# Performance work log

Measured on AMD Instinct MI355X. Metric: run time of the kernel, lower is better.

## Reference

```python
import jax, jax.numpy as jnp
import numpy as np

T = 4          # spiking time steps
HEADS = 12
SCALE = 0.125
TAU = 2.0
ALPHA = 4.0    # sigmoid surrogate sharpness
EPS = 1e-5

@jax.custom_vjp
def spike(x):
    # Heaviside forward, sigmoid surrogate backward (SigmoidGrad)
    return (x > 0).astype(x.dtype)

def _spike_fwd(x):
    return (x > 0).astype(x.dtype), x

def _spike_bwd(x, g):
    s = jax.nn.sigmoid(ALPHA * x)
    return (g * ALPHA * s * (1.0 - s),)

spike.defvjp(_spike_fwd, _spike_bwd)

def lif(x, threshold):
    # layer-by-layer LIF: x is [T*B, ...]; scan membrane over T steps
    TB = x.shape[0]
    B = TB // T
    xt = x.reshape((T, B) + x.shape[1:])
    def step(mem, xi):
        mem = mem + (xi - mem) / TAU
        s = spike(mem - threshold)
        mem = mem * (1.0 - jax.lax.stop_gradient(s))  # hard reset, spike detached
        return mem, s
    _, sp = jax.lax.scan(step, jnp.zeros_like(xt[0]), xt)
    return sp.reshape(x.shape)

def bn(x, p):
    # inference BatchNorm; p = [gamma, beta, mean, var] each [C], channel axis 1
    shape = (1, x.shape[1]) + (1,) * (x.ndim - 2)
    inv = jax.lax.rsqrt(p[3] + EPS)
    return (x - p[2].reshape(shape)) * (p[0] * inv).reshape(shape) + p[1].reshape(shape)

def setup_inputs() -> dict:
    key = jax.random.key(0)
    ks = jax.random.split(key, 9)
    C, HID, TB, H = 384, 1536, 128, 14
    return {
        'x': jax.random.normal(ks[0], (TB, C, H, H), jnp.float32),
        'qkvp_w': jax.random.normal(ks[1], (4, C, C), jnp.float32) * 0.05,
        'qkvp_bn': jax.random.uniform(ks[2], (4, 4, C), jnp.float32),
        'fc1_w': jax.random.normal(ks[3], (HID, C), jnp.float32) * 0.05,
        'fc1_b': jax.random.normal(ks[4], (HID,), jnp.float32) * 0.05,
        'fc1_bn': jax.random.uniform(ks[5], (4, HID), jnp.float32),
        'fc2_w': jax.random.normal(ks[6], (C, HID), jnp.float32) * 0.05,
        'fc2_b': jax.random.normal(ks[7], (C,), jnp.float32) * 0.05,
        'fc2_bn': jax.random.uniform(ks[8], (4, C), jnp.float32),
    }

def reference(x, qkvp_w, qkvp_bn, fc1_w, fc1_b, fc1_bn, fc2_w, fc2_b, fc2_bn):
    TB, C, H, W = x.shape
    N = H * W
    d = C // HEADS
    xf = x.reshape(TB, C, N)

    def branch(i):
        y = jnp.einsum('oc,bcn->bon', qkvp_w[i], xf)  # conv1d k=1, no bias
        y = lif(bn(y, qkvp_bn[i]), 1.0)
        # [TB,C,N] -> [TB,N,C] -> [TB,N,heads,d] -> [TB,heads,N,d]
        return y.transpose(0, 2, 1).reshape(TB, N, HEADS, d).transpose(0, 2, 1, 3)

    q, k, v = branch(0), branch(1), branch(2)
    attn = jnp.einsum('bhqd,bhkd->bhqk', q, k) * SCALE  # no softmax (spiking SSA)
    o = jnp.einsum('bhqk,bhkd->bhqd', attn, v)
    o = o.transpose(0, 1, 3, 2).reshape(TB, C, N)       # head-major channel layout
    o = lif(o, 0.5)                                     # attn_lif threshold=0.5
    o = jnp.einsum('oc,bcn->bon', qkvp_w[3], o)         # proj conv
    o = lif(bn(o, qkvp_bn[3]), 1.0).reshape(TB, C, H, W)

    x = x + o                                           # attention residual

    h = jnp.einsum('oc,bchw->bohw', fc1_w, x) + fc1_b[None, :, None, None]
    h = lif(bn(h, fc1_bn), 1.0)
    h = jnp.einsum('oc,bchw->bohw', fc2_w, h) + fc2_b[None, :, None, None]
    h = lif(bn(h, fc2_bn), 1.0)

    x = x + h                                           # MLP residual
    return (x, v)
```

## Files before the change

### kernel.cpp

```cpp
#include <hip/hip_runtime.h>
#include <hip/hip_bf16.h>


#define Cv 384
#define Nv 196
#define Mv 25088
#define HIDv 1536
#define Bv 32
#define Zv 6272
#define TBv 128
#define CHUNK 12544
#define UC 3136

__global__ __launch_bounds__(256) void k_transpose_in(const float* __restrict__ x,
                                                      float* __restrict__ xp)
{
    int idx = blockIdx.x * 256 + threadIdx.x;
    int c   = idx / Mv;
    int rem = idx - c * Mv;
    int z = rem >> 2, t = rem & 3;
    int b = z / Nv, n = z - b * Nv;
    xp[idx] = x[((size_t)(t * Bv + b) * Cv + c) * Nv + n];
}

__global__ __launch_bounds__(256) void k_gemm3(const float* __restrict__ W,
                                               const float* __restrict__ X,
                                               float* __restrict__ Y,
                                               int K, int ldx, int ldy,
                                               const float* __restrict__ bias,
                                               int cb)
{
    __shared__ float sW[16][68];
    __shared__ float sX[16][64];
    int ym0 = blockIdx.x * 64;
    int m0  = cb + ym0;
    int o0  = blockIdx.y * 64;
    int tid = threadIdx.x;
    int wo = tid & 63, wh = tid >> 6;
    int xr = tid >> 4, xc = (tid & 15) * 4;
    int to = tid >> 4, tm = tid & 15;

    const float* Wp = W + (size_t)(o0 + wo) * K + wh * 4;
    const float* Xp = X + (size_t)xr * ldx + m0 + xc;

    float acc[4][4];
    #pragma unroll
    for (int i = 0; i < 4; ++i)
        #pragma unroll
        for (int j = 0; j < 4; ++j) acc[i][j] = 0.0f;

    for (int k0 = 0; k0 < K; k0 += 16) {
        float4 w4 = *(const float4*)(Wp + k0);
        float4 x4 = *(const float4*)(Xp + (size_t)k0 * ldx);
        __syncthreads();
        sW[wh*4+0][wo] = w4.x;
        sW[wh*4+1][wo] = w4.y;
        sW[wh*4+2][wo] = w4.z;
        sW[wh*4+3][wo] = w4.w;
        *(float4*)&sX[xr][xc] = x4;
        __syncthreads();
        #pragma unroll
        for (int kk = 0; kk < 16; ++kk) {
            float4 a = *(const float4*)&sW[kk][to*4];
            float4 b = *(const float4*)&sX[kk][tm*4];
            float av[4] = {a.x, a.y, a.z, a.w};
            float bv[4] = {b.x, b.y, b.z, b.w};
            #pragma unroll
            for (int i = 0; i < 4; ++i)
                #pragma unroll
                for (int j = 0; j < 4; ++j)
                    acc[i][j] = fmaf(av[i], bv[j], acc[i][j]);
        }
    }
    #pragma unroll
    for (int i = 0; i < 4; ++i) {
        int o = o0 + to*4 + i;
        float bb = bias ? bias[o] : 0.0f;
        float4 r;
        r.x = acc[i][0] + bb; r.y = acc[i][1] + bb;
        r.z = acc[i][2] + bb; r.w = acc[i][3] + bb;
        *(float4*)&Y[(size_t)o * ldy + ym0 + tm*4] = r;
    }
}

__global__ __launch_bounds__(256) void k_vsse2(const float* __restrict__ W,
                                               const float* __restrict__ X,
                                               const float* __restrict__ bnp,
                                               __hip_bfloat16* __restrict__ Y)
{
    __shared__ float sW[32][68];
    __shared__ float sX[32][64];
    int m0 = blockIdx.x * 64;
    int o0 = blockIdx.y * 64;
    int tid = threadIdx.x;
    int to = tid >> 4, tm = tid & 15;

    float acc[4][4][4];
    #pragma unroll
    for (int s = 0; s < 4; ++s)
        #pragma unroll
        for (int op = 0; op < 4; ++op)
            #pragma unroll
            for (int e = 0; e < 4; ++e) acc[s][op][e] = 0.0f;

    int wq_o = tid >> 3, wq_c = tid & 7;
    int xs_r = tid >> 3, xs_c = (tid & 7) * 8;

    for (int blk = 0; blk < 12; ++blk) {
        int k0 = blk * 32;
        __syncthreads();
        {
            float4 w4 = *(const float4*)(W + (size_t)(o0 + wq_o) * Cv + k0 + wq_c*4);
            sW[wq_c*4+0][wq_o] = w4.x;
            sW[wq_c*4+1][wq_o] = w4.y;
            sW[wq_c*4+2][wq_o] = w4.z;
            sW[wq_c*4+3][wq_o] = w4.w;
            float4 w5 = *(const float4*)(W + (size_t)(o0 + 32 + wq_o) * Cv + k0 + wq_c*4);
            sW[wq_c*4+0][32 + wq_o] = w5.x;
            sW[wq_c*4+1][32 + wq_o] = w5.y;
            sW[wq_c*4+2][32 + wq_o] = w5.z;
            sW[wq_c*4+3][32 + wq_o] = w5.w;
        }
        {
            const float* Xp = X + (size_t)(k0 + xs_r) * Mv + m0 + xs_c;
            *(float4*)&sX[xs_r][xs_c]     = *(const float4*)(Xp);
            *(float4*)&sX[xs_r][xs_c + 4] = *(const float4*)(Xp + 4);
        }
        __syncthreads();
        #pragma unroll
        for (int j = 0; j < 8; ++j) {
            #pragma unroll
            for (int s = 0; s < 4; ++s) {
                int kk = j * 4 + s;
                float4 w4 = *(const float4*)&sW[kk][to*4];
                float4 x4 = *(const float4*)&sX[kk][tm*4];
                float wv[4] = {w4.x, w4.y, w4.z, w4.w};
                float xv[4] = {x4.x, x4.y, x4.z, x4.w};
                #pragma unroll
                for (int op = 0; op < 4; ++op)
                    #pragma unroll
                    for (int e = 0; e < 4; ++e)
                        acc[s][op][e] = __fadd_rn(acc[s][op][e],
                                                  __fmul_rn(wv[op], xv[e]));
            }
        }
    }

    #pragma unroll
    for (int op = 0; op < 4; ++op) {
        int o = o0 + to*4 + op;
        float inv = __fdiv_rn(1.0f, __fsqrt_rn(__fadd_rn(bnp[3*Cv + o], 1e-5f)));
        float sc  = __fmul_rn(bnp[o], inv);
        float mu  = bnp[2*Cv + o];
        float be  = bnp[Cv + o];
        float mem = 0.0f;
        ushort4 pk;
        unsigned short* pks = (unsigned short*)&pk;
        #pragma unroll
        for (int e = 0; e < 4; ++e) {
            float tot = __fadd_rn(__fadd_rn(acc[0][op][e], acc[2][op][e]),
                                  __fadd_rn(acc[1][op][e], acc[3][op][e]));
            float bn = __fadd_rn(__fmul_rn(__fsub_rn(tot, mu), sc), be);
            mem = __fadd_rn(mem, __fmul_rn(__fsub_rn(bn, mem), 0.5f));
            int s = (mem > 1.0f);
            mem = s ? 0.0f : mem;
            pks[e] = s ? 0x3F80 : 0;
        }
        *(ushort4*)((unsigned short*)Y + (size_t)o * Mv + m0 + tm * 4) = pk;
    }
}

__global__ __launch_bounds__(256) void k_bnlif_spike(const float* __restrict__ y,
                                                     const float* __restrict__ bnp,
                                                     __hip_bfloat16* __restrict__ sp)
{
    int idx = blockIdx.x * 256 + threadIdx.x;
    int c = idx / Zv;
    float gamma = bnp[c], beta = bnp[Cv+c], mean = bnp[2*Cv+c], var = bnp[3*Cv+c];
    float scale = gamma / sqrtf(var + 1e-5f);
    size_t base = (size_t)idx * 4;
    float4 yv = *(const float4*)(y + base);
    float xi[4] = {yv.x, yv.y, yv.z, yv.w};
    ushort4 pk;
    unsigned short* pks = (unsigned short*)&pk;
    float mem = 0.f;
    #pragma unroll
    for (int t = 0; t < 4; ++t) {
        float xv = (xi[t] - mean) * scale + beta;
        mem = mem + (xv - mem) * 0.5f;
        float s = (mem > 1.0f) ? 1.0f : 0.0f;
        mem *= (1.0f - s);
        pks[t] = (s > 0.5f) ? 0x3F80 : 0;
    }
    *(ushort4*)((unsigned short*)sp + base) = pk;
}

__global__ __launch_bounds__(256) void k_attn(const __hip_bfloat16* __restrict__ qs,
                                              const __hip_bfloat16* __restrict__ ks,
                                              const __hip_bfloat16* __restrict__ vs,
                                              float* __restrict__ o_chan,
                                              float* __restrict__ v_out)
{
    int h = blockIdx.x, tbl = blockIdx.y;
    int t = tbl >> 5, b = tbl & 31;
    int tid = threadIdx.x;
    __shared__ unsigned kmask[196];
    __shared__ float vf[196][36];
    size_t chb  = (size_t)h * 32 * Mv;
    size_t colb = (size_t)b * Nv * 4 + t;

    for (int e = tid; e < Nv * 32; e += 256) {
        int dd = e / Nv, n = e - dd * Nv;
        vf[n][dd] = __bfloat162float(vs[chb + (size_t)dd * Mv + colb + (size_t)n * 4]);
    }
    unsigned qm = 0;
    if (tid < Nv) {
        unsigned km = 0;
        #pragma unroll
        for (int dd = 0; dd < 32; ++dd) {
            size_t off = chb + (size_t)dd * Mv + colb + (size_t)tid * 4;
            km |= (__bfloat162float(ks[off]) > 0.5f ? 1u : 0u) << dd;
            qm |= (__bfloat162float(qs[off]) > 0.5f ? 1u : 0u) << dd;
        }
        kmask[tid] = km;
    }
    __syncthreads();
    for (int e = tid; e < Nv * 32; e += 256) {
        int n = e >> 5, dd = e & 31;
        v_out[((size_t)(tbl * 12 + h) * Nv + n) * 32 + dd] = vf[n][dd];
    }
    if (tid < Nv) {
        float acc[32] = {};
        for (int nk = 0; nk < Nv; ++nk) {
            float a = (float)__popc(qm & kmask[nk]) * 0.125f;
            #pragma unroll
            for (int dd = 0; dd < 32; ++dd) acc[dd] += a * vf[nk][dd];
        }
        #pragma unroll
        for (int dd = 0; dd < 32; ++dd)
            o_chan[chb + (size_t)dd * Mv + colb + (size_t)tid * 4] = acc[dd];
    }
}

__global__ __launch_bounds__(256) void k_attnlif(float* __restrict__ o)
{
    int idx = blockIdx.x * 256 + threadIdx.x;
    size_t base = (size_t)idx * 4;
    float4 v = *(const float4*)(o + base);
    float xi[4] = {v.x, v.y, v.z, v.w};
    float s4[4];
    float mem = 0.f;
    #pragma unroll
    for (int t = 0; t < 4; ++t) {
        mem = mem + (xi[t] - mem) * 0.5f;
        s4[t] = (mem > 0.5f) ? 1.0f : 0.0f;
        mem *= (1.0f - s4[t]);
    }
    float4 r; r.x = s4[0]; r.y = s4[1]; r.z = s4[2]; r.w = s4[3];
    *(float4*)(o + base) = r;
}

__global__ __launch_bounds__(256) void k_resid(const float* __restrict__ p,
                                               const float* __restrict__ bnp,
                                               float* __restrict__ x1,
                                               __hip_bfloat16* __restrict__ s_proj)
{
    int idx = blockIdx.x * 256 + threadIdx.x;
    int c = idx / Zv;
    float gamma = bnp[c], beta = bnp[Cv+c], mean = bnp[2*Cv+c], var = bnp[3*Cv+c];
    float scale = gamma / sqrtf(var + 1e-5f);
    size_t base = (size_t)idx * 4;
    float4 pv = *(const float4*)(p + base);
    float xi[4] = {pv.x, pv.y, pv.z, pv.w};
    float4 xv = *(const float4*)(x1 + base);
    float xr[4] = {xv.x, xv.y, xv.z, xv.w};
    ushort4 pk;
    unsigned short* pks = (unsigned short*)&pk;
    float mem = 0.f;
    #pragma unroll
    for (int t = 0; t < 4; ++t) {
        float bnv = (xi[t] - mean) * scale + beta;
        mem = mem + (bnv - mem) * 0.5f;
        float s = (mem > 1.0f) ? 1.0f : 0.0f;
        mem *= (1.0f - s);
        xr[t] += s;
        pks[t] = (s > 0.5f) ? 0x3F80 : 0;
    }
    float4 r; r.x = xr[0]; r.y = xr[1]; r.z = xr[2]; r.w = xr[3];
    *(float4*)(x1 + base) = r;
    *(ushort4*)((unsigned short*)s_proj + base) = pk;
}

__global__ __launch_bounds__(256) void k_bnlif_h(float* __restrict__ hbuf,
                                                 const float* __restrict__ bnp)
{
    int idx = blockIdx.x * 256 + threadIdx.x;
    int o = idx / UC;
    float gamma = bnp[o], beta = bnp[HIDv+o], mean = bnp[2*HIDv+o], var = bnp[3*HIDv+o];
    float scale = gamma / sqrtf(var + 1e-5f);
    size_t base = (size_t)idx * 4;
    float4 hv = *(const float4*)(hbuf + base);
    float xi[4] = {hv.x, hv.y, hv.z, hv.w};
    float s4[4];
    float mem = 0.f;
    #pragma unroll
    for (int t = 0; t < 4; ++t) {
        float bnv = (xi[t] - mean) * scale + beta;
        mem = mem + (bnv - mem) * 0.5f;
        s4[t] = (mem > 1.0f) ? 1.0f : 0.0f;
        mem *= (1.0f - s4[t]);
    }
    float4 r; r.x = s4[0]; r.y = s4[1]; r.z = s4[2]; r.w = s4[3];
    *(float4*)(hbuf + base) = r;
}

__global__ __launch_bounds__(256) void k_final(const float* __restrict__ h2,
                                               const float* __restrict__ bnp,
                                               const float* __restrict__ x,
                                               const __hip_bfloat16* __restrict__ s_proj,
                                               float* __restrict__ out,
                                               int b0)
{
    int idx = blockIdx.x * 256 + threadIdx.x;
    int c = idx / UC;
    int u = idx - c * UC;
    int bp = u / Nv, n = u - bp * Nv;
    int b = b0 + bp;
    float gamma = bnp[c], beta = bnp[Cv+c], mean = bnp[2*Cv+c], var = bnp[3*Cv+c];
    float scale = gamma / sqrtf(var + 1e-5f);
    float4 hv = *(const float4*)(h2 + (size_t)c * CHUNK + (size_t)u * 4);
    float xi[4] = {hv.x, hv.y, hv.z, hv.w};
    ushort4 sp4 = *(const ushort4*)((const unsigned short*)s_proj +
                                    (size_t)c * Mv + ((size_t)b * Nv + n) * 4);
    unsigned short* sps = (unsigned short*)&sp4;
    float mem = 0.f;
    #pragma unroll
    for (int t = 0; t < 4; ++t) {
        float bnv = (xi[t] - mean) * scale + beta;
        mem = mem + (bnv - mem) * 0.5f;
        float s = (mem > 1.0f) ? 1.0f : 0.0f;
        mem *= (1.0f - s);
        size_t oidx = ((size_t)(t * Bv + b) * Cv + c) * Nv + n;
        float sproj = sps[t] ? 1.0f : 0.0f;
        out[oidx] = x[oidx] + sproj + s;
    }
}

extern "C" void kernel_launch(void* const* d_in, const int* in_sizes, int n_in,
                              void* d_out, int out_size, void* d_ws, size_t ws_size,
                              hipStream_t stream)
{
    const float* x       = (const float*)d_in[0];
    const float* qkvp_w  = (const float*)d_in[1];
    const float* qkvp_bn = (const float*)d_in[2];
    const float* fc1_w   = (const float*)d_in[3];
    const float* fc1_b   = (const float*)d_in[4];
    const float* fc1_bn  = (const float*)d_in[5];
    const float* fc2_w   = (const float*)d_in[6];
    const float* fc2_b   = (const float*)d_in[7];
    const float* fc2_bn  = (const float*)d_in[8];

    float* out1 = (float*)d_out;
    float* out2 = out1 + (size_t)TBv * Cv * Nv;

    float* wsf = (float*)d_ws;
    const size_t S = (size_t)Cv * Mv;
    if (ws_size < 4 * S * sizeof(float)) return;

    float* xp   = wsf;
    float* ybuf = wsf + S;
    __hip_bfloat16* qs = (__hip_bfloat16*)(wsf + 2*S);
    __hip_bfloat16* ks = qs + S;
    __hip_bfloat16* vs = qs + 2*S;
    float* pbuf  = wsf + 2*S;
    float* hbuf  = wsf + S;
    float* h2buf = wsf + 3*S;
    __hip_bfloat16* s_proj = (__hip_bfloat16*)(wsf + 3*S + S/2);

    k_transpose_in<<<37632, 256, 0, stream>>>(x, xp);

    for (int br = 0; br < 2; ++br) {
        k_gemm3<<<dim3(392, 6), 256, 0, stream>>>(qkvp_w + (size_t)br*Cv*Cv, xp, ybuf,
                                                  Cv, Mv, Mv, nullptr, 0);
        __hip_bfloat16* sp = (br == 0) ? qs : ks;
        k_bnlif_spike<<<9408, 256, 0, stream>>>(ybuf, qkvp_bn + (size_t)br*4*Cv, sp);
    }
    k_vsse2<<<dim3(392, 6), 256, 0, stream>>>(qkvp_w + (size_t)2*Cv*Cv, xp,
                                              qkvp_bn + (size_t)2*4*Cv, vs);

    k_attn<<<dim3(12, 128), 256, 0, stream>>>(qs, ks, vs, ybuf, out2);
    k_attnlif<<<9408, 256, 0, stream>>>(ybuf);

    k_gemm3<<<dim3(392, 6), 256, 0, stream>>>(qkvp_w + (size_t)3*Cv*Cv, ybuf, pbuf,
                                              Cv, Mv, Mv, nullptr, 0);
    k_resid<<<9408, 256, 0, stream>>>(pbuf, qkvp_bn + (size_t)3*4*Cv, xp, s_proj);

    for (int ch = 0; ch < 2; ++ch) {
        k_gemm3<<<dim3(196, 24), 256, 0, stream>>>(fc1_w, xp, hbuf,
                                                   Cv, Mv, CHUNK, fc1_b, ch * CHUNK);
        k_bnlif_h<<<18816, 256, 0, stream>>>(hbuf, fc1_bn);
        k_gemm3<<<dim3(196, 6), 256, 0, stream>>>(fc2_w, hbuf, h2buf,
                                                  HIDv, CHUNK, CHUNK, fc2_b, 0);
        k_final<<<4704, 256, 0, stream>>>(h2buf, fc2_bn, x, s_proj, out1, ch * 16);
    }
}
```

Baseline: 1.450 ms.

## Fuse fc1 with BN+LIF into bf16 spikes, widen GEMM tiles, drop MLP chunking

Replaces the 64x64 fp32 GEMM with a 64x128 tile variant that can read bf16 inputs. fc1 now applies bias, BatchNorm and LIF in its epilogue and writes bf16 spikes directly. This removes the separate bnlif pass and the full fp32 hidden-activation round trip. With the smaller hidden buffer the MLP runs in one pass instead of two chunks, and the workspace layout is reorganised to fit. The larger accumulator tile raises register pressure and may lower occupancy.

```diff
diff --git a/kernel.cpp b/kernel.cpp
--- a/kernel.cpp
+++ b/kernel.cpp
@@ -9,8 +9,6 @@
 #define Bv 32
 #define Zv 6272
 #define TBv 128
-#define CHUNK 12544
-#define UC 3136
 
 __global__ __launch_bounds__(256) void k_transpose_in(const float* __restrict__ x,
                                                       float* __restrict__ xp)
@@ -23,52 +21,70 @@
     xp[idx] = x[((size_t)(t * Bv + b) * Cv + c) * Nv + n];
 }
 
-__global__ __launch_bounds__(256) void k_gemm3(const float* __restrict__ W,
-                                               const float* __restrict__ X,
+template<int XBF16>
+__global__ __launch_bounds__(256) void k_gemm4(const float* __restrict__ W,
+                                               const void* __restrict__ Xv,
                                                float* __restrict__ Y,
                                                int K, int ldx, int ldy,
                                                const float* __restrict__ bias,
                                                int cb)
 {
     __shared__ float sW[16][68];
-    __shared__ float sX[16][64];
-    int ym0 = blockIdx.x * 64;
+    __shared__ float sX[16][128];
+    int ym0 = blockIdx.x * 128;
     int m0  = cb + ym0;
     int o0  = blockIdx.y * 64;
     int tid = threadIdx.x;
     int wo = tid & 63, wh = tid >> 6;
-    int xr = tid >> 4, xc = (tid & 15) * 4;
+    int xr = tid >> 4, xc = (tid & 15) * 8;
     int to = tid >> 4, tm = tid & 15;
 
     const float* Wp = W + (size_t)(o0 + wo) * K + wh * 4;
-    const float* Xp = X + (size_t)xr * ldx + m0 + xc;
-
-    float acc[4][4];
+
+    float acc[4][8];
     #pragma unroll
     for (int i = 0; i < 4; ++i)
         #pragma unroll
-        for (int j = 0; j < 4; ++j) acc[i][j] = 0.0f;
+        for (int j = 0; j < 8; ++j) acc[i][j] = 0.0f;
 
     for (int k0 = 0; k0 < K; k0 += 16) {
         float4 w4 = *(const float4*)(Wp + k0);
-        float4 x4 = *(const float4*)(Xp + (size_t)k0 * ldx);
+        float xf[8];
+        if (XBF16) {
+            const unsigned short* Xb = (const unsigned short*)Xv;
+            uint4 u = *(const uint4*)(Xb + (size_t)(k0 + xr) * ldx + m0 + xc);
+            unsigned uu[4] = {u.x, u.y, u.z, u.w};
+            #pragma unroll
+            for (int q = 0; q < 4; ++q) {
+                xf[2*q]   = __uint_as_float((uu[q] & 0xFFFFu) << 16);
+                xf[2*q+1] = __uint_as_float(uu[q] & 0xFFFF0000u);
+            }
+        } else {
+            const float* Xf = (const float*)Xv;
+            float4 xa = *(const float4*)(Xf + (size_t)(k0 + xr) * ldx + m0 + xc);
+            float4 xb = *(const float4*)(Xf + (size_t)(k0 + xr) * ldx + m0 + xc + 4);
+            xf[0]=xa.x; xf[1]=xa.y; xf[2]=xa.z; xf[3]=xa.w;
+            xf[4]=xb.x; xf[5]=xb.y; xf[6]=xb.z; xf[7]=xb.w;
+        }
         __syncthreads();
         sW[wh*4+0][wo] = w4.x;
         sW[wh*4+1][wo] = w4.y;
         sW[wh*4+2][wo] = w4.z;
         sW[wh*4+3][wo] = w4.w;
-        *(float4*)&sX[xr][xc] = x4;
+        *(float4*)&sX[xr][xc]     = *(float4*)&xf[0];
+        *(float4*)&sX[xr][xc + 4] = *(float4*)&xf[4];
         __syncthreads();
         #pragma unroll
         for (int kk = 0; kk < 16; ++kk) {
-            float4 a = *(const float4*)&sW[kk][to*4];
-            float4 b = *(const float4*)&sX[kk][tm*4];
+            float4 a  = *(const float4*)&sW[kk][to*4];
+            float4 b0 = *(const float4*)&sX[kk][tm*4];
+            float4 b1 = *(const float4*)&sX[kk][64 + tm*4];
             float av[4] = {a.x, a.y, a.z, a.w};
-            float bv[4] = {b.x, b.y, b.z, b.w};
+            float bv[8] = {b0.x,b0.y,b0.z,b0.w,b1.x,b1.y,b1.z,b1.w};
             #pragma unroll
             for (int i = 0; i < 4; ++i)
                 #pragma unroll
-                for (int j = 0; j < 4; ++j)
+                for (int j = 0; j < 8; ++j)
                     acc[i][j] = fmaf(av[i], bv[j], acc[i][j]);
         }
     }
@@ -76,10 +92,88 @@
     for (int i = 0; i < 4; ++i) {
         int o = o0 + to*4 + i;
         float bb = bias ? bias[o] : 0.0f;
-        float4 r;
-        r.x = acc[i][0] + bb; r.y = acc[i][1] + bb;
-        r.z = acc[i][2] + bb; r.w = acc[i][3] + bb;
-        *(float4*)&Y[(size_t)o * ldy + ym0 + tm*4] = r;
+        float4 r0, r1;
+        r0.x = acc[i][0] + bb; r0.y = acc[i][1] + bb;
+        r0.z = acc[i][2] + bb; r0.w = acc[i][3] + bb;
+        r1.x = acc[i][4] + bb; r1.y = acc[i][5] + bb;
+        r1.z = acc[i][6] + bb; r1.w = acc[i][7] + bb;
+        *(float4*)&Y[(size_t)o * ldy + ym0 + tm*4]      = r0;
+        *(float4*)&Y[(size_t)o * ldy + ym0 + 64 + tm*4] = r1;
+    }
+}
+
+__global__ __launch_bounds__(256) void k_fc1(const float* __restrict__ W,
+                                             const float* __restrict__ X,
+                                             const float* __restrict__ bias,
+                                             const float* __restrict__ bnp,
+                                             __hip_bfloat16* __restrict__ H)
+{
+    __shared__ float sW[16][68];
+    __shared__ float sX[16][128];
+    int ym0 = blockIdx.x * 128;
+    int o0  = blockIdx.y * 64;
+    int tid = threadIdx.x;
+    int wo = tid & 63, wh = tid >> 6;
+    int xr = tid >> 4, xc = (tid & 15) * 8;
+    int to = tid >> 4, tm = tid & 15;
+
+    const float* Wp = W + (size_t)(o0 + wo) * Cv + wh * 4;
+
+    float acc[4][8];
+    #pragma unroll
+    for (int i = 0; i < 4; ++i)
+        #pragma unroll
+        for (int j = 0; j < 8; ++j) acc[i][j] = 0.0f;
+
+    for (int k0 = 0; k0 < Cv; k0 += 16) {
+        float4 w4 = *(const float4*)(Wp + k0);
+        float4 xa = *(const float4*)(X + (size_t)(k0 + xr) * Mv + ym0 + xc);
+        float4 xb = *(const float4*)(X + (size_t)(k0 + xr) * Mv + ym0 + xc + 4);
+        __syncthreads();
+        sW[wh*4+0][wo] = w4.x;
+        sW[wh*4+1][wo] = w4.y;
+        sW[wh*4+2][wo] = w4.z;
+        sW[wh*4+3][wo] = w4.w;
+        *(float4*)&sX[xr][xc]     = xa;
+        *(float4*)&sX[xr][xc + 4] = xb;
+        __syncthreads();
+        #pragma unroll
+        for (int kk = 0; kk < 16; ++kk) {
+            float4 a  = *(const float4*)&sW[kk][to*4];
+            float4 b0 = *(const float4*)&sX[kk][tm*4];
+            float4 b1 = *(const float4*)&sX[kk][64 + tm*4];
+            float av[4] = {a.x, a.y, a.z, a.w};
+            float bv[8] = {b0.x,b0.y,b0.z,b0.w,b1.x,b1.y,b1.z,b1.w};
+            #pragma unroll
+            for (int i = 0; i < 4; ++i)
+                #pragma unroll
+                for (int j = 0; j < 8; ++j)
+                    acc[i][j] = fmaf(av[i], bv[j], acc[i][j]);
+        }
+    }
+    #pragma unroll
+    for (int i = 0; i < 4; ++i) {
+        int o = o0 + to*4 + i;
+        float inv = __fdiv_rn(1.0f, __fsqrt_rn(__fadd_rn(bnp[3*HIDv + o], 1e-5f)));
+        float sc  = __fmul_rn(bnp[o], inv);
+        float mu  = bnp[2*HIDv + o];
+        float be  = bnp[HIDv + o];
+        #pragma unroll
+        for (int half = 0; half < 2; ++half) {
+            float mem = 0.0f;
+            ushort4 pk;
+            unsigned short* pks = (unsigned short*)&pk;
+            #pragma unroll
+            for (int t = 0; t < 4; ++t) {
+                float val = __fadd_rn(acc[i][half*4 + t], bias[o]);
+                float bn  = __fadd_rn(__fmul_rn(__fsub_rn(val, mu), sc), be);
+                mem = __fadd_rn(mem, __fmul_rn(__fsub_rn(bn, mem), 0.5f));
+                int s = (mem > 1.0f);
+                mem = s ? 0.0f : mem;
+                pks[t] = s ? 0x3F80 : 0;
+            }
+            *(ushort4*)((unsigned short*)H + (size_t)o * Mv + ym0 + half*64 + tm*4) = pk;
+        }
     }
 }
 
@@ -291,47 +385,22 @@
     *(ushort4*)((unsigned short*)s_proj + base) = pk;
 }
 
-__global__ __launch_bounds__(256) void k_bnlif_h(float* __restrict__ hbuf,
-                                                 const float* __restrict__ bnp)
-{
-    int idx = blockIdx.x * 256 + threadIdx.x;
-    int o = idx / UC;
-    float gamma = bnp[o], beta = bnp[HIDv+o], mean = bnp[2*HIDv+o], var = bnp[3*HIDv+o];
-    float scale = gamma / sqrtf(var + 1e-5f);
-    size_t base = (size_t)idx * 4;
-    float4 hv = *(const float4*)(hbuf + base);
-    float xi[4] = {hv.x, hv.y, hv.z, hv.w};
-    float s4[4];
-    float mem = 0.f;
-    #pragma unroll
-    for (int t = 0; t < 4; ++t) {
-        float bnv = (xi[t] - mean) * scale + beta;
-        mem = mem + (bnv - mem) * 0.5f;
-        s4[t] = (mem > 1.0f) ? 1.0f : 0.0f;
-        mem *= (1.0f - s4[t]);
-    }
-    float4 r; r.x = s4[0]; r.y = s4[1]; r.z = s4[2]; r.w = s4[3];
-    *(float4*)(hbuf + base) = r;
-}
-
 __global__ __launch_bounds__(256) void k_final(const float* __restrict__ h2,
                                                const float* __restrict__ bnp,
                                                const float* __restrict__ x,
                                                const __hip_bfloat16* __restrict__ s_proj,
-                                               float* __restrict__ out,
-                                               int b0)
+                                               float* __restrict__ out)
 {
     int idx = blockIdx.x * 256 + threadIdx.x;
-    int c = idx / UC;
-    int u = idx - c * UC;
-    int bp = u / Nv, n = u - bp * Nv;
-    int b = b0 + bp;
+    int c = idx / Zv;
+    int z = idx - c * Zv;
+    int b = z / Nv, n = z - b * Nv;
     float gamma = bnp[c], beta = bnp[Cv+c], mean = bnp[2*Cv+c], var = bnp[3*Cv+c];
     float scale = gamma / sqrtf(var + 1e-5f);
-    float4 hv = *(const float4*)(h2 + (size_t)c * CHUNK + (size_t)u * 4);
+    size_t base = (size_t)idx * 4;
+    float4 hv = *(const float4*)(h2 + base);
     float xi[4] = {hv.x, hv.y, hv.z, hv.w};
-    ushort4 sp4 = *(const ushort4*)((const unsigned short*)s_proj +
-                                    (size_t)c * Mv + ((size_t)b * Nv + n) * 4);
+    ushort4 sp4 = *(const ushort4*)((const unsigned short*)s_proj + base);
     unsigned short* sps = (unsigned short*)&sp4;
     float mem = 0.f;
     #pragma unroll
@@ -363,44 +432,43 @@
     float* out1 = (float*)d_out;
     float* out2 = out1 + (size_t)TBv * Cv * Nv;
 
-    float* wsf = (float*)d_ws;
-    const size_t S = (size_t)Cv * Mv;
-    if (ws_size < 4 * S * sizeof(float)) return;
-
-    float* xp   = wsf;
-    float* ybuf = wsf + S;
-    __hip_bfloat16* qs = (__hip_bfloat16*)(wsf + 2*S);
-    __hip_bfloat16* ks = qs + S;
-    __hip_bfloat16* vs = qs + 2*S;
-    float* pbuf  = wsf + 2*S;
-    float* hbuf  = wsf + S;
-    float* h2buf = wsf + 3*S;
-    __hip_bfloat16* s_proj = (__hip_bfloat16*)(wsf + 3*S + S/2);
-
-    k_transpose_in<<<37632, 256, 0, stream>>>(x, xp);
+    const size_t S  = (size_t)Cv * Mv;
+    const size_t S4 = S * 4;
+    if (ws_size < 4 * S4) return;
+
+    char* wb = (char*)d_ws;
+    float* xp            = (float*)wb;
+    float* ybuf          = (float*)(wb + S4);
+    __hip_bfloat16* qs   = (__hip_bfloat16*)(wb + 2*S4);
+    __hip_bfloat16* ks   = (__hip_bfloat16*)(wb + 2*S4 + S4/2);
+    __hip_bfloat16* vs   = (__hip_bfloat16*)(wb + 3*S4);
+    float* pbuf          = (float*)(wb + 2*S4);
+    __hip_bfloat16* s_pr = (__hip_bfloat16*)(wb + 3*S4 + S4/2);
+    __hip_bfloat16* H    = (__hip_bfloat16*)(wb + S4);
+    float* h2            = (float*)wb;
+
+    k_transpose_in<<<(int)(S/256), 256, 0, stream>>>(x, xp);
 
     for (int br = 0; br < 2; ++br) {
-        k_gemm3<<<dim3(392, 6), 256, 0, stream>>>(qkvp_w + (size_t)br*Cv*Cv, xp, ybuf,
-                                                  Cv, Mv, Mv, nullptr, 0);
+        k_gemm4<0><<<dim3(196, 6), 256, 0, stream>>>(qkvp_w + (size_t)br*Cv*Cv, xp,
+                                                     ybuf, Cv, Mv, Mv, nullptr, 0);
         __hip_bfloat16* sp = (br == 0) ? qs : ks;
-        k_bnlif_spike<<<9408, 256, 0, stream>>>(ybuf, qkvp_bn + (size_t)br*4*Cv, sp);
+        k_bnlif_spike<<<(int)(S/1024), 256, 0, stream>>>(ybuf, qkvp_bn + (size_t)br*4*Cv, sp);
     }
     k_vsse2<<<dim3(392, 6), 256, 0, stream>>>(qkvp_w + (size_t)2*Cv*Cv, xp,
                                               qkvp_bn + (size_t)2*4*Cv, vs);
 
     k_attn<<<dim3(12, 128), 256, 0, stream>>>(qs, ks, vs, ybuf, out2);
-    k_attnlif<<<9408, 256, 0, stream>>>(ybuf);
-
-    k_gemm3<<<dim3(392, 6), 256, 0, stream>>>(qkvp_w + (size_t)3*Cv*Cv, ybuf, pbuf,
-                                              Cv, Mv, Mv, nullptr, 0);
-    k_resid<<<9408, 256, 0, stream>>>(pbuf, qkvp_bn + (size_t)3*4*Cv, xp, s_proj);
-
-    for (int ch = 0; ch < 2; ++ch) {
-        k_gemm3<<<dim3(196, 24), 256, 0, stream>>>(fc1_w, xp, hbuf,
-                                                   Cv, Mv, CHUNK, fc1_b, ch * CHUNK);
-        k_bnlif_h<<<18816, 256, 0, stream>>>(hbuf, fc1_bn);
-        k_gemm3<<<dim3(196, 6), 256, 0, stream>>>(fc2_w, hbuf, h2buf,
-                                                  HIDv, CHUNK, CHUNK, fc2_b, 0);
-        k_final<<<4704, 256, 0, stream>>>(h2buf, fc2_bn, x, s_proj, out1, ch * 16);
-    }
-}
+    k_attnlif<<<(int)(S/1024), 256, 0, stream>>>(ybuf);
+
+    k_gemm4<0><<<dim3(196, 6), 256, 0, stream>>>(qkvp_w + (size_t)3*Cv*Cv, ybuf,
+                                                 pbuf, Cv, Mv, Mv, nullptr, 0);
+    k_resid<<<(int)(S/1024), 256, 0, stream>>>(pbuf, qkvp_bn + (size_t)3*4*Cv, xp, s_pr);
+
+    k_fc1<<<dim3(196, 24), 256, 0, stream>>>(fc1_w, xp, fc1_b, fc1_bn, H);
+
+    k_gemm4<1><<<dim3(196, 6), 256, 0, stream>>>(fc2_w, H, h2,
+                                                 HIDv, Mv, Mv, fc2_b, 0);
+
+    k_final<<<(int)(S/1024), 256, 0, stream>>>(h2, fc2_bn, x, s_pr, out1);
+}
```

Measured after the change: 1.366 ms. -5.8%, faster.

## Fuse BN+LIF epilogues into a templated GEMM and drop intermediate elementwise kernels

Applied to the files above, without the earlier changes.

Replaces the shared-memory tiled GEMM with a templated kernel that stages only X in LDS, reads W per wavefront from global/scalar memory, and applies BN+LIF spiking directly in the epilogue, writing bf16 spikes. The separate bnlif, resid and bnlif_h kernels go away: the attention residual is folded into the fc1 GEMM's input load, and the fc1 hidden activations are stored as bf16 spikes that fc2 reads. The MLP no longer runs in two chunks. This cuts full-tensor fp32 round trips and launches. The cost is that W is read through uniform per-wave loads instead of LDS, which may be less efficient.

```diff
diff --git a/kernel.cpp b/kernel.cpp
--- a/kernel.cpp
+++ b/kernel.cpp
@@ -9,8 +9,6 @@
 #define Bv 32
 #define Zv 6272
 #define TBv 128
-#define CHUNK 12544
-#define UC 3136
 
 __global__ __launch_bounds__(256) void k_transpose_in(const float* __restrict__ x,
                                                       float* __restrict__ xp)
@@ -23,63 +21,108 @@
     xp[idx] = x[((size_t)(t * Bv + b) * Cv + c) * Nv + n];
 }
 
-__global__ __launch_bounds__(256) void k_gemm3(const float* __restrict__ W,
-                                               const float* __restrict__ X,
-                                               float* __restrict__ Y,
-                                               int K, int ldx, int ldy,
+template<int XBF16, int SADD, int BIAS, int EPI>
+__global__ __launch_bounds__(256) void k_gemm5(const float* __restrict__ W,
+                                               const void* __restrict__ Xv,
+                                               const __hip_bfloat16* __restrict__ Xs,
                                                const float* __restrict__ bias,
-                                               int cb)
-{
-    __shared__ float sW[16][68];
-    __shared__ float sX[16][64];
-    int ym0 = blockIdx.x * 64;
-    int m0  = cb + ym0;
-    int o0  = blockIdx.y * 64;
-    int tid = threadIdx.x;
-    int wo = tid & 63, wh = tid >> 6;
-    int xr = tid >> 4, xc = (tid & 15) * 4;
-    int to = tid >> 4, tm = tid & 15;
-
-    const float* Wp = W + (size_t)(o0 + wo) * K + wh * 4;
-    const float* Xp = X + (size_t)xr * ldx + m0 + xc;
-
-    float acc[4][4];
-    #pragma unroll
-    for (int i = 0; i < 4; ++i)
+                                               const float* __restrict__ bnp,
+                                               int bnC,
+                                               void* __restrict__ Y,
+                                               int K)
+{
+    __shared__ float sX[8][256];
+    int tid  = threadIdx.x;
+    int lane = tid & 63;
+    int wid  = __builtin_amdgcn_readfirstlane(tid >> 6);
+    int m0   = blockIdx.x * 256;
+    int ob   = blockIdx.y * 32 + wid * 8;
+    int mL   = m0 + lane * 4;
+    int sr   = tid >> 5;
+    int sc   = (tid & 31) * 8;
+
+    float acc[8][4];
+    #pragma unroll
+    for (int i = 0; i < 8; ++i)
         #pragma unroll
         for (int j = 0; j < 4; ++j) acc[i][j] = 0.0f;
 
-    for (int k0 = 0; k0 < K; k0 += 16) {
-        float4 w4 = *(const float4*)(Wp + k0);
-        float4 x4 = *(const float4*)(Xp + (size_t)k0 * ldx);
+    for (int k0 = 0; k0 < K; k0 += 8) {
+        float xf[8];
+        if (XBF16) {
+            const unsigned short* Xb = (const unsigned short*)Xv;
+            uint4 u = *(const uint4*)(Xb + (size_t)(k0 + sr) * Mv + m0 + sc);
+            unsigned uu[4] = {u.x, u.y, u.z, u.w};
+            #pragma unroll
+            for (int q = 0; q < 4; ++q) {
+                xf[2*q]   = __uint_as_float((uu[q] & 0xFFFFu) << 16);
+                xf[2*q+1] = __uint_as_float(uu[q] & 0xFFFF0000u);
+            }
+        } else {
+            const float* Xf = (const float*)Xv;
+            float4 xa = *(const float4*)(Xf + (size_t)(k0 + sr) * Mv + m0 + sc);
+            float4 xb = *(const float4*)(Xf + (size_t)(k0 + sr) * Mv + m0 + sc + 4);
+            xf[0]=xa.x; xf[1]=xa.y; xf[2]=xa.z; xf[3]=xa.w;
+            xf[4]=xb.x; xf[5]=xb.y; xf[6]=xb.z; xf[7]=xb.w;
+            if (SADD) {
+                uint4 u = *(const uint4*)((const unsigned short*)Xs +
+                                          (size_t)(k0 + sr) * Mv + m0 + sc);
+                unsigned uu[4] = {u.x, u.y, u.z, u.w};
+                #pragma unroll
+                for (int q = 0; q < 4; ++q) {
+                    xf[2*q]   = __fadd_rn(xf[2*q],   (uu[q] & 0xFFFFu)      ? 1.0f : 0.0f);
+                    xf[2*q+1] = __fadd_rn(xf[2*q+1], (uu[q] & 0xFFFF0000u) ? 1.0f : 0.0f);
+                }
+            }
+        }
         __syncthreads();
-        sW[wh*4+0][wo] = w4.x;
-        sW[wh*4+1][wo] = w4.y;
-        sW[wh*4+2][wo] = w4.z;
-        sW[wh*4+3][wo] = w4.w;
-        *(float4*)&sX[xr][xc] = x4;
+        *(float4*)&sX[sr][sc]     = *(float4*)&xf[0];
+        *(float4*)&sX[sr][sc + 4] = *(float4*)&xf[4];
         __syncthreads();
-        #pragma unroll
-        for (int kk = 0; kk < 16; ++kk) {
-            float4 a = *(const float4*)&sW[kk][to*4];
-            float4 b = *(const float4*)&sX[kk][tm*4];
-            float av[4] = {a.x, a.y, a.z, a.w};
-            float bv[4] = {b.x, b.y, b.z, b.w};
-            #pragma unroll
-            for (int i = 0; i < 4; ++i)
+        const float* Wb = W + (size_t)ob * K + k0;
+        #pragma unroll
+        for (int kk = 0; kk < 8; ++kk) {
+            float4 xq = *(const float4*)&sX[kk][lane * 4];
+            float xv[4] = {xq.x, xq.y, xq.z, xq.w};
+            #pragma unroll
+            for (int i = 0; i < 8; ++i) {
+                float wv = Wb[(size_t)i * K + kk];
                 #pragma unroll
                 for (int j = 0; j < 4; ++j)
-                    acc[i][j] = fmaf(av[i], bv[j], acc[i][j]);
-        }
-    }
-    #pragma unroll
-    for (int i = 0; i < 4; ++i) {
-        int o = o0 + to*4 + i;
-        float bb = bias ? bias[o] : 0.0f;
-        float4 r;
-        r.x = acc[i][0] + bb; r.y = acc[i][1] + bb;
-        r.z = acc[i][2] + bb; r.w = acc[i][3] + bb;
-        *(float4*)&Y[(size_t)o * ldy + ym0 + tm*4] = r;
+                    acc[i][j] = fmaf(wv, xv[j], acc[i][j]);
+            }
+        }
+    }
+
+    #pragma unroll
+    for (int i = 0; i < 8; ++i) {
+        int o = ob + i;
+        if (EPI == 0) {
+            float bb = BIAS ? bias[o] : 0.0f;
+            float4 r;
+            r.x = acc[i][0] + bb; r.y = acc[i][1] + bb;
+            r.z = acc[i][2] + bb; r.w = acc[i][3] + bb;
+            *(float4*)((float*)Y + (size_t)o * Mv + mL) = r;
+        } else {
+            float inv = __fdiv_rn(1.0f, __fsqrt_rn(__fadd_rn(bnp[3*bnC + o], 1e-5f)));
+            float scl = __fmul_rn(bnp[o], inv);
+            float mu  = bnp[2*bnC + o];
+            float be  = bnp[bnC + o];
+            float mem = 0.0f;
+            ushort4 pk;
+            unsigned short* pks = (unsigned short*)&pk;
+            #pragma unroll
+            for (int j = 0; j < 4; ++j) {
+                float val = acc[i][j];
+                if (BIAS) val = __fadd_rn(val, bias[o]);
+                float bn = __fadd_rn(__fmul_rn(__fsub_rn(val, mu), scl), be);
+                mem = __fadd_rn(mem, __fmul_rn(__fsub_rn(bn, mem), 0.5f));
+                int s = (mem > 1.0f);
+                mem = s ? 0.0f : mem;
+                pks[j] = s ? 0x3F80 : 0;
+            }
+            *(ushort4*)((unsigned short*)Y + (size_t)o * Mv + mL) = pk;
+        }
     }
 }
 
@@ -170,31 +213,6 @@
     }
 }
 
-__global__ __launch_bounds__(256) void k_bnlif_spike(const float* __restrict__ y,
-                                                     const float* __restrict__ bnp,
-                                                     __hip_bfloat16* __restrict__ sp)
-{
-    int idx = blockIdx.x * 256 + threadIdx.x;
-    int c = idx / Zv;
-    float gamma = bnp[c], beta = bnp[Cv+c], mean = bnp[2*Cv+c], var = bnp[3*Cv+c];
-    float scale = gamma / sqrtf(var + 1e-5f);
-    size_t base = (size_t)idx * 4;
-    float4 yv = *(const float4*)(y + base);
-    float xi[4] = {yv.x, yv.y, yv.z, yv.w};
-    ushort4 pk;
-    unsigned short* pks = (unsigned short*)&pk;
-    float mem = 0.f;
-    #pragma unroll
-    for (int t = 0; t < 4; ++t) {
-        float xv = (xi[t] - mean) * scale + beta;
-        mem = mem + (xv - mem) * 0.5f;
-        float s = (mem > 1.0f) ? 1.0f : 0.0f;
-        mem *= (1.0f - s);
-        pks[t] = (s > 0.5f) ? 0x3F80 : 0;
-    }
-    *(ushort4*)((unsigned short*)sp + base) = pk;
-}
-
 __global__ __launch_bounds__(256) void k_attn(const __hip_bfloat16* __restrict__ qs,
                                               const __hip_bfloat16* __restrict__ ks,
                                               const __hip_bfloat16* __restrict__ vs,
@@ -260,78 +278,22 @@
     *(float4*)(o + base) = r;
 }
 
-__global__ __launch_bounds__(256) void k_resid(const float* __restrict__ p,
-                                               const float* __restrict__ bnp,
-                                               float* __restrict__ x1,
-                                               __hip_bfloat16* __restrict__ s_proj)
-{
-    int idx = blockIdx.x * 256 + threadIdx.x;
-    int c = idx / Zv;
-    float gamma = bnp[c], beta = bnp[Cv+c], mean = bnp[2*Cv+c], var = bnp[3*Cv+c];
-    float scale = gamma / sqrtf(var + 1e-5f);
-    size_t base = (size_t)idx * 4;
-    float4 pv = *(const float4*)(p + base);
-    float xi[4] = {pv.x, pv.y, pv.z, pv.w};
-    float4 xv = *(const float4*)(x1 + base);
-    float xr[4] = {xv.x, xv.y, xv.z, xv.w};
-    ushort4 pk;
-    unsigned short* pks = (unsigned short*)&pk;
-    float mem = 0.f;
-    #pragma unroll
-    for (int t = 0; t < 4; ++t) {
-        float bnv = (xi[t] - mean) * scale + beta;
-        mem = mem + (bnv - mem) * 0.5f;
-        float s = (mem > 1.0f) ? 1.0f : 0.0f;
-        mem *= (1.0f - s);
-        xr[t] += s;
-        pks[t] = (s > 0.5f) ? 0x3F80 : 0;
-    }
-    float4 r; r.x = xr[0]; r.y = xr[1]; r.z = xr[2]; r.w = xr[3];
-    *(float4*)(x1 + base) = r;
-    *(ushort4*)((unsigned short*)s_proj + base) = pk;
-}
-
-__global__ __launch_bounds__(256) void k_bnlif_h(float* __restrict__ hbuf,
-                                                 const float* __restrict__ bnp)
-{
-    int idx = blockIdx.x * 256 + threadIdx.x;
-    int o = idx / UC;
-    float gamma = bnp[o], beta = bnp[HIDv+o], mean = bnp[2*HIDv+o], var = bnp[3*HIDv+o];
-    float scale = gamma / sqrtf(var + 1e-5f);
-    size_t base = (size_t)idx * 4;
-    float4 hv = *(const float4*)(hbuf + base);
-    float xi[4] = {hv.x, hv.y, hv.z, hv.w};
-    float s4[4];
-    float mem = 0.f;
-    #pragma unroll
-    for (int t = 0; t < 4; ++t) {
-        float bnv = (xi[t] - mean) * scale + beta;
-        mem = mem + (bnv - mem) * 0.5f;
-        s4[t] = (mem > 1.0f) ? 1.0f : 0.0f;
-        mem *= (1.0f - s4[t]);
-    }
-    float4 r; r.x = s4[0]; r.y = s4[1]; r.z = s4[2]; r.w = s4[3];
-    *(float4*)(hbuf + base) = r;
-}
-
 __global__ __launch_bounds__(256) void k_final(const float* __restrict__ h2,
                                                const float* __restrict__ bnp,
                                                const float* __restrict__ x,
                                                const __hip_bfloat16* __restrict__ s_proj,
-                                               float* __restrict__ out,
-                                               int b0)
+                                               float* __restrict__ out)
 {
     int idx = blockIdx.x * 256 + threadIdx.x;
-    int c = idx / UC;
-    int u = idx - c * UC;
-    int bp = u / Nv, n = u - bp * Nv;
-    int b = b0 + bp;
+    int c = idx / Zv;
+    int z = idx - c * Zv;
+    int b = z / Nv, n = z - b * Nv;
     float gamma = bnp[c], beta = bnp[Cv+c], mean = bnp[2*Cv+c], var = bnp[3*Cv+c];
     float scale = gamma / sqrtf(var + 1e-5f);
-    float4 hv = *(const float4*)(h2 + (size_t)c * CHUNK + (size_t)u * 4);
+    size_t base = (size_t)idx * 4;
+    float4 hv = *(const float4*)(h2 + base);
     float xi[4] = {hv.x, hv.y, hv.z, hv.w};
-    ushort4 sp4 = *(const ushort4*)((const unsigned short*)s_proj +
-                                    (size_t)c * Mv + ((size_t)b * Nv + n) * 4);
+    ushort4 sp4 = *(const ushort4*)((const unsigned short*)s_proj + base);
     unsigned short* sps = (unsigned short*)&sp4;
     float mem = 0.f;
     #pragma unroll
@@ -363,44 +325,40 @@
     float* out1 = (float*)d_out;
     float* out2 = out1 + (size_t)TBv * Cv * Nv;
 
-    float* wsf = (float*)d_ws;
-    const size_t S = (size_t)Cv * Mv;
-    if (ws_size < 4 * S * sizeof(float)) return;
-
-    float* xp   = wsf;
-    float* ybuf = wsf + S;
-    __hip_bfloat16* qs = (__hip_bfloat16*)(wsf + 2*S);
-    __hip_bfloat16* ks = qs + S;
-    __hip_bfloat16* vs = qs + 2*S;
-    float* pbuf  = wsf + 2*S;
-    float* hbuf  = wsf + S;
-    float* h2buf = wsf + 3*S;
-    __hip_bfloat16* s_proj = (__hip_bfloat16*)(wsf + 3*S + S/2);
-
-    k_transpose_in<<<37632, 256, 0, stream>>>(x, xp);
-
-    for (int br = 0; br < 2; ++br) {
-        k_gemm3<<<dim3(392, 6), 256, 0, stream>>>(qkvp_w + (size_t)br*Cv*Cv, xp, ybuf,
-                                                  Cv, Mv, Mv, nullptr, 0);
-        __hip_bfloat16* sp = (br == 0) ? qs : ks;
-        k_bnlif_spike<<<9408, 256, 0, stream>>>(ybuf, qkvp_bn + (size_t)br*4*Cv, sp);
-    }
+    const size_t S  = (size_t)Cv * Mv;
+    const size_t S4 = S * 4;
+    if (ws_size < 4 * S4) return;
+
+    char* wb = (char*)d_ws;
+    float* xp            = (float*)wb;
+    float* obuf          = (float*)(wb + S4);
+    __hip_bfloat16* qs   = (__hip_bfloat16*)(wb + 2*S4);
+    __hip_bfloat16* ks   = (__hip_bfloat16*)(wb + 2*S4 + S4/2);
+    __hip_bfloat16* vs   = (__hip_bfloat16*)(wb + 3*S4);
+    __hip_bfloat16* s_pr = (__hip_bfloat16*)(wb + 3*S4 + S4/2);
+    __hip_bfloat16* H    = (__hip_bfloat16*)(wb + S4);
+    float* h2            = (float*)wb;
+
+    k_transpose_in<<<(int)(S/256), 256, 0, stream>>>(x, xp);
+
+    k_gemm5<0,0,0,1><<<dim3(98, 12), 256, 0, stream>>>(
+        qkvp_w, xp, nullptr, nullptr, qkvp_bn, Cv, qs, Cv);
+    k_gemm5<0,0,0,1><<<dim3(98, 12), 256, 0, stream>>>(
+        qkvp_w + (size_t)Cv*Cv, xp, nullptr, nullptr, qkvp_bn + 4*Cv, Cv, ks, Cv);
     k_vsse2<<<dim3(392, 6), 256, 0, stream>>>(qkvp_w + (size_t)2*Cv*Cv, xp,
                                               qkvp_bn + (size_t)2*4*Cv, vs);
 
-    k_attn<<<dim3(12, 128), 256, 0, stream>>>(qs, ks, vs, ybuf, out2);
-    k_attnlif<<<9408, 256, 0, stream>>>(ybuf);
-
-    k_gemm3<<<dim3(392, 6), 256, 0, stream>>>(qkvp_w + (size_t)3*Cv*Cv, ybuf, pbuf,
-                                              Cv, Mv, Mv, nullptr, 0);
-    k_resid<<<9408, 256, 0, stream>>>(pbuf, qkvp_bn + (size_t)3*4*Cv, xp, s_proj);
-
-    for (int ch = 0; ch < 2; ++ch) {
-        k_gemm3<<<dim3(196, 24), 256, 0, stream>>>(fc1_w, xp, hbuf,
-                                                   Cv, Mv, CHUNK, fc1_b, ch * CHUNK);
-        k_bnlif_h<<<18816, 256, 0, stream>>>(hbuf, fc1_bn);
-        k_gemm3<<<dim3(196, 6), 256, 0, stream>>>(fc2_w, hbuf, h2buf,
-                                                  HIDv, CHUNK, CHUNK, fc2_b, 0);
-        k_final<<<4704, 256, 0, stream>>>(h2buf, fc2_bn, x, s_proj, out1, ch * 16);
-    }
-}
+    k_attn<<<dim3(12, 128), 256, 0, stream>>>(qs, ks, vs, obuf, out2);
+    k_attnlif<<<(int)(S/1024), 256, 0, stream>>>(obuf);
+
+    k_gemm5<0,0,0,1><<<dim3(98, 12), 256, 0, stream>>>(
+        qkvp_w + (size_t)3*Cv*Cv, obuf, nullptr, nullptr, qkvp_bn + 3*4*Cv, Cv, s_pr, Cv);
+
+    k_gemm5<0,1,1,1><<<dim3(98, 48), 256, 0, stream>>>(
+        fc1_w, xp, s_pr, fc1_b, fc1_bn, HIDv, H, Cv);
+
+    k_gemm5<1,0,1,0><<<dim3(98, 12), 256, 0, stream>>>(
+        fc2_w, H, nullptr, fc2_b, nullptr, 0, h2, HIDv);
+
+    k_final<<<(int)(S/1024), 256, 0, stream>>>(h2, fc2_bn, x, s_pr, out1);
+}
```

After: 1.244 ms. -14.2%, faster.
